# Optimization experiments

Hardware: AMD Instinct MI355X
Metric: run time of the kernel (lower is better)

## Reference

```python
import jax, jax.numpy as jnp
import numpy as np
from jax import lax

J = 3  # number of decomposition levels
SQ2 = float(1.0 / np.sqrt(2.0))


def _corr(Xp, hr, axis, Lout, stride):
    """Strided valid correlation of padded Xp with taps hr along `axis`.
    out[n] = sum_k hr[k] * Xp[n*stride + k]. Tap loop is over <=10 static taps."""
    m = hr.shape[0]
    hi = stride * (Lout - 1) + 1
    acc = hr[0] * lax.slice_in_dim(Xp, 0, hi, stride, axis)
    for k in range(1, m):
        acc = acc + hr[k] * lax.slice_in_dim(Xp, k, k + hi, stride, axis)
    return acc


def colfilter(X, h):
    # 'same' convolution along H with symmetric (edge-repeat) extension.
    m = h.shape[0]; m2 = m // 2; L = X.shape[2]
    Xp = jnp.pad(X, ((0, 0), (0, 0), (m2, m2), (0, 0)), mode='symmetric')
    return _corr(Xp, h[::-1], 2, L, 1)  # corr with reversed taps == convolution


def rowfilter(X, h):
    m = h.shape[0]; m2 = m // 2; L = X.shape[3]
    Xp = jnp.pad(X, ((0, 0), (0, 0), (0, 0), (m2, m2)), mode='symmetric')
    return _corr(Xp, h[::-1], 3, L, 1)


def coldfilt(X, ha, hb, highpass):
    # Dual-tree decimated (by 2) filtering along H. r must be a multiple of 4.
    b, c, r, w = X.shape
    m = ha.shape[0]; r4 = r // 4
    Xp = jnp.pad(X, ((0, 0), (0, 0), (m, m), (0, 0)), mode='symmetric')
    E = Xp[:, :, 2::2, :]  # even-phase stream, len r/2+m-1
    O = Xp[:, :, 3::2, :]  # odd-phase stream
    a_out = _corr(O, ha[::-1], 2, r4, 2)
    b_out = _corr(E, hb[::-1], 2, r4, 2)
    ev, od = (b_out, a_out) if highpass else (a_out, b_out)
    return jnp.stack([ev, od], axis=3).reshape(b, c, r // 2, w)


def rowdfilt(X, ha, hb, highpass):
    b, c, r, w = X.shape
    m = ha.shape[0]; w4 = w // 4
    Xp = jnp.pad(X, ((0, 0), (0, 0), (0, 0), (m, m)), mode='symmetric')
    E = Xp[:, :, :, 2::2]
    O = Xp[:, :, :, 3::2]
    a_out = _corr(O, ha[::-1], 3, w4, 2)
    b_out = _corr(E, hb[::-1], 3, w4, 2)
    ev, od = (b_out, a_out) if highpass else (a_out, b_out)
    return jnp.stack([ev, od], axis=4).reshape(b, c, r, w // 2)


def q2c(y):
    # Convert quads of real pixels into two complex subbands.
    y = y * SQ2
    a = y[..., 0::2, 0::2]; b = y[..., 0::2, 1::2]
    c = y[..., 1::2, 0::2]; d = y[..., 1::2, 1::2]
    return (a - d, b + c), (a + d, b - c)


def _bands(lh, hh, hl):
    # Orientation order [15, 45, 75, 105, 135, 165] deg; real/imag in last dim.
    (r15, i15), (r165, i165) = q2c(lh)
    (r45, i45), (r135, i135) = q2c(hh)
    (r75, i75), (r105, i105) = q2c(hl)
    c = lambda re, im: jnp.stack([re, im], axis=-1)
    return jnp.stack([c(r15, i15), c(r45, i45), c(r75, i75),
                      c(r105, i105), c(r135, i135), c(r165, i165)], axis=2)


def dtcwt_forward(x, h0o, h1o, h0a, h0b, h1a, h1b):
    # Level 1 (undecimated biorthogonal filters; q2c decimates bandpass by 2).
    lo = rowfilter(x, h0o)
    hi = rowfilter(x, h1o)
    ll = colfilter(lo, h0o)
    yh = [_bands(colfilter(lo, h1o), colfilter(hi, h1o), colfilter(hi, h0o))]
    # Levels 2..J (quarter-shift dual-tree decimated filters).
    for _ in range(1, J):
        lo = rowdfilt(ll, h0b, h0a, False)
        hi = rowdfilt(ll, h1b, h1a, True)
        lh = coldfilt(lo, h1b, h1a, True)
        hl = coldfilt(hi, h0b, h0a, False)
        hh = coldfilt(hi, h1b, h1a, True)
        ll = coldfilt(lo, h0b, h0a, False)
        yh.append(_bands(lh, hh, hl))
    return (ll, yh[0], yh[1], yh[2])


def _filters():
    h0o = np.array([-0.05, 0.25, 0.6, 0.25, -0.05], dtype=np.float32)
    h1o = np.array([-3/280, 3/56, 73/280, -17/28, 73/280, 3/56, -3/280],
                   dtype=np.float32)
    h0a = np.array([0.03516384, 0.0, -0.08832942, 0.23389032, 0.76027237,
                    0.58751830, 0.0, -0.11430184, 0.0, 0.0], dtype=np.float32)
    h0b = h0a[::-1].copy()
    alt = ((-1.0) ** np.arange(10)).astype(np.float32)
    h1a = h0b * alt
    h1b = h1a[::-1].copy()
    return {k: jnp.asarray(v) for k, v in dict(
        h0o=h0o, h1o=h1o, h0a=h0a, h0b=h0b, h1a=h1a, h1b=h1b).items()}


def setup_inputs() -> dict:
    key = jax.random.key(0)
    x = jax.random.normal(key, (8, 16, 256, 256), dtype=jnp.float32)
    inp = {'x': x}
    inp.update(_filters())
    return inp


def reference(x, h0o, h1o, h0a, h0b, h1a, h1b):
    return dtcwt_forward(x, h0o, h1o, h0a, h0b, h1a, h1b)
```

## Files before the change

### kernel.cpp

```cpp
#include <hip/hip_runtime.h>

#define SQ2F 0.70710678118654752440f

static constexpr float H0O[5] = {-0.05f, 0.25f, 0.6f, 0.25f, -0.05f};
static constexpr float H1O[7] = {(float)(-3.0/280.0), (float)(3.0/56.0), (float)(73.0/280.0),
                                 (float)(-17.0/28.0), (float)(73.0/280.0), (float)(3.0/56.0),
                                 (float)(-3.0/280.0)};
static constexpr float H0A[10] = {0.03516384f, 0.0f, -0.08832942f, 0.23389032f, 0.76027237f,
                                  0.5875183f, 0.0f, -0.11430184f, 0.0f, 0.0f};
static constexpr float H0B[10] = {0.0f, 0.0f, -0.11430184f, 0.0f, 0.5875183f,
                                  0.76027237f, 0.23389032f, -0.08832942f, 0.0f, 0.03516384f};
static constexpr float H1A[10] = {0.0f, 0.0f, -0.11430184f, 0.0f, 0.5875183f,
                                  -0.76027237f, 0.23389032f, 0.08832942f, 0.0f, -0.03516384f};
static constexpr float H1B[10] = {-0.03516384f, 0.0f, 0.08832942f, 0.23389032f, -0.76027237f,
                                  0.5875183f, 0.0f, -0.11430184f, 0.0f, 0.0f};

__device__ __forceinline__ int symref(int t, int L) {
    if (t < 0) t = -1 - t;
    if (t >= L) t = 2 * L - 1 - t;
    return t;
}

__device__ __forceinline__ void gload_lds4(const float* g, float* lds) {
    __builtin_amdgcn_global_load_lds(
        (const __attribute__((address_space(1))) void*)g,
        (__attribute__((address_space(3))) void*)lds, 4, 0, 0);
}

#define XS(r,c)  S[(r)*84 + (c)]
#define LS(r,c)  S[(r)*85 + (c)]
#define LOS(r,c) S[4368 + (r)*80 + (c)]
#define LO2(r,c) S[4368 + (r)*33 + (c)]
#define HI2(r,c) S[5952 + (r)*33 + (c)]
#define HIS(r,c) S[8528 + (r)*64 + (c)]

__global__ __launch_bounds__(512) void dtcwt_l12(
    const float* __restrict__ x,
    float* __restrict__ yh0,
    float* __restrict__ yh1,
    float* __restrict__ ll2)
{
    __shared__ float S[10960];
    int tid = threadIdx.x, bx = blockIdx.x;
    int tj = bx & 3, ti = (bx >> 2) & 7, bc = bx >> 5;
    const int xr0 = 32 * ti - 10, xc0 = 64 * tj - 10;
    const float* xb = x + (size_t)bc * 65536;
    const int lane = tid & 63;

    const bool interior0 = (ti >= 1) && (ti <= 6) && (tj >= 1) && (tj <= 2);
    if (interior0) {
        for (int p = tid; p < 4368; p += 512) {
            int r = p / 84, c = p - r * 84;
            gload_lds4(xb + (xr0 + r) * 256 + (xc0 + c), &S[p - lane]);
        }
    } else {
        for (int p = tid; p < 4368; p += 512) {
            int r = p / 84, c = p - r * 84;
            gload_lds4(xb + symref(xr0 + r, 256) * 256 + symref(xc0 + c, 256),
                       &S[p - lane]);
        }
    }
    __syncthreads();

    for (int p = tid; p < 4160; p += 512) {
        int r = p / 80, c = p - r * 80;
        float l = 0.f;
        #pragma unroll
        for (int t = 0; t < 5; t++) l += H0O[t] * XS(r, c + 4 - t);
        LOS(r, c) = l;
    }
    for (int p = tid; p < 2432; p += 512) {
        int r = p >> 6, c = p & 63;
        float h = 0.f;
        #pragma unroll
        for (int t = 0; t < 7; t++) h += H1O[t] * XS(r + 7, c + 13 - t);
        HIS(r, c) = h;
    }
    __syncthreads();

    for (int p = tid; p < 3840; p += 512) {
        int r = p / 80, c = p - r * 80;
        float v = 0.f;
        #pragma unroll
        for (int t = 0; t < 5; t++) v += H0O[t] * LOS(r + 4 - t, c);
        LS(r, c) = v;
    }
    {
        float* yb = yh0 + (size_t)bc * 196608;
        const size_t bs = 32768;
        int par = lane & 1;
        #pragma unroll
        for (int it = 0; it < 2; ++it) {
            int oi = (tid >> 6) + 8 * it;
            float low[8], hiw[8];
            #pragma unroll
            for (int k = 0; k < 8; k++) {
                low[k] = LOS(2 * oi + 7 + k, lane + 8);
                hiw[k] = HIS(2 * oi + k,     lane);
            }
            float lh_e = 0, lh_o = 0, hh_e = 0, hh_o = 0, hl_e = 0, hl_o = 0;
            #pragma unroll
            for (int t = 0; t < 7; t++) {
                lh_e += H1O[t] * low[6 - t]; lh_o += H1O[t] * low[7 - t];
                hh_e += H1O[t] * hiw[6 - t]; hh_o += H1O[t] * hiw[7 - t];
            }
            #pragma unroll
            for (int t = 0; t < 5; t++) {
                hl_e += H0O[t] * hiw[5 - t]; hl_o += H0O[t] * hiw[6 - t];
            }
            lh_e *= SQ2F; lh_o *= SQ2F; hh_e *= SQ2F; hh_o *= SQ2F; hl_e *= SQ2F; hl_o *= SQ2F;
            float p0 = lh_e - __shfl_xor(lh_o, 1), q0 = __shfl_xor(lh_e, 1) + lh_o;
            float p1 = hh_e - __shfl_xor(hh_o, 1), q1 = __shfl_xor(hh_e, 1) + hh_o;
            float p2 = hl_e - __shfl_xor(hl_o, 1), q2 = __shfl_xor(hl_e, 1) + hl_o;
            int i0 = 16 * ti + oi, j0 = 32 * tj + (lane >> 1);
            size_t pix = ((size_t)i0 * 128 + j0) * 2;
            *(float2*)&yb[(size_t)(par ? 5 : 0) * bs + pix] =
                par ? make_float2(q0, p0) : make_float2(p0, q0);
            *(float2*)&yb[(size_t)(par ? 4 : 1) * bs + pix] =
                par ? make_float2(q1, p1) : make_float2(p1, q1);
            *(float2*)&yb[(size_t)(par ? 3 : 2) * bs + pix] =
                par ? make_float2(q2, p2) : make_float2(p2, q2);
        }
    }
    __syncthreads();

    {
        const bool interiorC = (tj >= 1) && (tj <= 2);
        for (int p = tid; p < 768; p += 512) {
            int r = p % 48, nl = p / 48;
            float v[20];
            if (interiorC) {
                #pragma unroll
                for (int k = 0; k < 20; k++) v[k] = LS(r, 4 * nl + k);
            } else {
                int gcb = 64 * tj + 4 * nl - 8;
                #pragma unroll
                for (int k = 0; k < 20; k++)
                    v[k] = LS(r, symref(gcb + k, 256) - 64 * tj + 8);
            }
            float aLo = 0.f, bLo = 0.f, aHi = 0.f, bHi = 0.f;
            #pragma unroll
            for (int t = 0; t < 10; t++) {
                float vo = v[19 - 2 * t], ve = v[18 - 2 * t];
                aLo += H0B[t] * vo; bLo += H0A[t] * ve;
                aHi += H1B[t] * vo; bHi += H1A[t] * ve;
            }
            LO2(r, 2*nl)   = aLo;
            LO2(r, 2*nl+1) = bLo;
            HI2(r, 2*nl)   = bHi;
            HI2(r, 2*nl+1) = aHi;
        }
    }
    __syncthreads();

    if (tid < 256) {
        int c  = tid & 31;
        int li = tid >> 5;
        int i1 = 8 * ti + li;
        float vl[20], vh[20];
        const bool interiorR = (ti >= 1) && (ti <= 6);
        if (interiorR) {
            #pragma unroll
            for (int k = 0; k < 20; k++) {
                vl[k] = LO2(4 * li + k, c);
                vh[k] = HI2(4 * li + k, c);
            }
        } else {
            #pragma unroll
            for (int k = 0; k < 20; k++) {
                int loc = symref(32 * ti + 4 * li - 8 + k, 256) - 32 * ti + 8;
                vl[k] = LO2(loc, c);
                vh[k] = HI2(loc, c);
            }
        }
        float a_ll=0,b_ll=0,a_lh=0,b_lh=0,a_hl=0,b_hl=0,a_hh=0,b_hh=0;
        #pragma unroll
        for (int t = 0; t < 10; t++) {
            float vo_l = vl[19 - 2*t], ve_l = vl[18 - 2*t];
            float vo_h = vh[19 - 2*t], ve_h = vh[18 - 2*t];
            a_ll += H0B[t] * vo_l;  b_ll += H0A[t] * ve_l;
            a_lh += H1B[t] * vo_l;  b_lh += H1A[t] * ve_l;
            a_hl += H0B[t] * vo_h;  b_hl += H0A[t] * ve_h;
            a_hh += H1B[t] * vo_h;  b_hh += H1A[t] * ve_h;
        }
        float* llb = ll2 + (size_t)bc * 16384;
        int gcol = 32 * tj + c;
        llb[(size_t)(2*i1)   * 128 + gcol] = a_ll;
        llb[(size_t)(2*i1+1) * 128 + gcol] = b_ll;
        float lh_e = SQ2F*b_lh, lh_o = SQ2F*a_lh;
        float hh_e = SQ2F*b_hh, hh_o = SQ2F*a_hh;
        float hl_e = SQ2F*a_hl, hl_o = SQ2F*b_hl;
        int par = c & 1;
        float p0 = lh_e - __shfl_xor(lh_o, 1), q0 = __shfl_xor(lh_e, 1) + lh_o;
        float p1 = hh_e - __shfl_xor(hh_o, 1), q1 = __shfl_xor(hh_e, 1) + hh_o;
        float p2 = hl_e - __shfl_xor(hl_o, 1), q2 = __shfl_xor(hl_e, 1) + hl_o;
        float* yb = yh1 + (size_t)bc * 49152;
        int j1 = 16 * tj + (c >> 1);
        size_t pix = ((size_t)i1 * 64 + j1) * 2;
        const size_t bs = 8192;
        *(float2*)&yb[(size_t)(par ? 5 : 0) * bs + pix] =
            par ? make_float2(q0, p0) : make_float2(p0, q0);
        *(float2*)&yb[(size_t)(par ? 4 : 1) * bs + pix] =
            par ? make_float2(q1, p1) : make_float2(p1, q1);
        *(float2*)&yb[(size_t)(par ? 3 : 2) * bs + pix] =
            par ? make_float2(q2, p2) : make_float2(p2, q2);
    }
}

__global__ __launch_bounds__(256) void level_fused(
    const float* __restrict__ X,
    float* __restrict__ llout,
    float* __restrict__ yh,
    int R, int C, int nbi, int nbj)
{
    __shared__ float Xs[80][81];
    __shared__ float Lo[80][33];
    __shared__ float Hi[80][33];

    int tid = threadIdx.x;
    int bx  = blockIdx.x;
    int tj = bx % nbj; int ti = (bx / nbj) % nbi; int bc = bx / (nbj * nbi);
    int i0 = ti * 16, j0 = tj * 16;
    int gr0 = 4 * i0 - 8, gc0 = 4 * j0 - 8;
    const float* Xb = X + (size_t)bc * R * C;

    for (int p = tid; p < 80 * 80; p += 256) {
        int r = p / 80, c = p - r * 80;
        Xs[r][c] = Xb[(size_t)symref(gr0 + r, R) * C + symref(gc0 + c, C)];
    }
    __syncthreads();

    for (int p = tid; p < 80 * 16; p += 256) {
        int nl = p / 80, r = p - nl * 80;
        float v[20];
        #pragma unroll
        for (int k = 0; k < 20; k++) v[k] = Xs[r][4 * nl + k];
        float aLo = 0.f, bLo = 0.f, aHi = 0.f, bHi = 0.f;
        #pragma unroll
        for (int t = 0; t < 10; t++) {
            float vo = v[19 - 2 * t], ve = v[18 - 2 * t];
            aLo += H0B[t] * vo; bLo += H0A[t] * ve;
            aHi += H1B[t] * vo; bHi += H1A[t] * ve;
        }
        Lo[r][2*nl]   = aLo;
        Lo[r][2*nl+1] = bLo;
        Hi[r][2*nl]   = bHi;
        Hi[r][2*nl+1] = aHi;
    }
    __syncthreads();

    int R4 = R >> 2, Wq = C >> 2, C2 = C >> 1;
    int lj = tid & 15, li = tid >> 4;
    int i = i0 + li, j = j0 + lj;

    float ll_[2][2], lh_[2][2], hl_[2][2], hh_[2][2];
    #pragma unroll
    for (int cc = 0; cc < 2; cc++) {
        int c = 2 * lj + cc;
        float vl[20], vh[20];
        #pragma unroll
        for (int k = 0; k < 20; k++) {
            vl[k] = Lo[4 * li + k][c];
            vh[k] = Hi[4 * li + k][c];
        }
        float a_ll=0,b_ll=0,a_lh=0,b_lh=0,a_hl=0,b_hl=0,a_hh=0,b_hh=0;
        #pragma unroll
        for (int t = 0; t < 10; t++) {
            float vo_l = vl[19 - 2*t], ve_l = vl[18 - 2*t];
            float vo_h = vh[19 - 2*t], ve_h = vh[18 - 2*t];
            a_ll += H0B[t] * vo_l;  b_ll += H0A[t] * ve_l;
            a_lh += H1B[t] * vo_l;  b_lh += H1A[t] * ve_l;
            a_hl += H0B[t] * vo_h;  b_hl += H0A[t] * ve_h;
            a_hh += H1B[t] * vo_h;  b_hh += H1A[t] * ve_h;
        }
        ll_[0][cc] = a_ll; ll_[1][cc] = b_ll;
        lh_[0][cc] = b_lh; lh_[1][cc] = a_lh;
        hl_[0][cc] = a_hl; hl_[1][cc] = b_hl;
        hh_[0][cc] = b_hh; hh_[1][cc] = a_hh;
    }

    float* llb = llout + (size_t)bc * (R >> 1) * C2;
    llb[(size_t)(2*i)*C2   + 2*j]     = ll_[0][0];
    llb[(size_t)(2*i)*C2   + 2*j + 1] = ll_[0][1];
    llb[(size_t)(2*i+1)*C2 + 2*j]     = ll_[1][0];
    llb[(size_t)(2*i+1)*C2 + 2*j + 1] = ll_[1][1];

    float* yb = yh + (size_t)bc * 6 * R4 * Wq * 2;
    size_t pix = ((size_t)i * Wq + j) * 2;
    size_t bs  = (size_t)R4 * Wq * 2;
    {
        float a = SQ2F*lh_[0][0], b = SQ2F*lh_[0][1], c = SQ2F*lh_[1][0], d = SQ2F*lh_[1][1];
        yb[0*bs + pix] = a - d; yb[0*bs + pix + 1] = b + c;
        yb[5*bs + pix] = a + d; yb[5*bs + pix + 1] = b - c;
    }
    {
        float a = SQ2F*hh_[0][0], b = SQ2F*hh_[0][1], c = SQ2F*hh_[1][0], d = SQ2F*hh_[1][1];
        yb[1*bs + pix] = a - d; yb[1*bs + pix + 1] = b + c;
        yb[4*bs + pix] = a + d; yb[4*bs + pix + 1] = b - c;
    }
    {
        float a = SQ2F*hl_[0][0], b = SQ2F*hl_[0][1], c = SQ2F*hl_[1][0], d = SQ2F*hl_[1][1];
        yb[2*bs + pix] = a - d; yb[2*bs + pix + 1] = b + c;
        yb[3*bs + pix] = a + d; yb[3*bs + pix + 1] = b - c;
    }
}

extern "C" void kernel_launch(void* const* d_in, const int* in_sizes, int n_in,
                              void* d_out, int out_size, void* d_ws, size_t ws_size,
                              hipStream_t stream) {
    const float* x = (const float*)d_in[0];
    float* out = (float*)d_out;

    const int BC = 8 * 16;

    float* out_ll  = out;
    float* out_yh0 = out + 524288;
    float* out_yh1 = out + 25690112;
    float* out_yh2 = out + 31981568;

    float* ll2 = (float*)d_ws;

    dtcwt_l12<<<BC * 32, 512, 0, stream>>>(x, out_yh0, out_yh1, ll2);

    level_fused<<<BC * 4, 256, 0, stream>>>(ll2, out_ll, out_yh2, 128, 128, 2, 2);
}
```

Measured before the change: 209.7 us.

## Vectorize LDS filtering with register blocking and drop boundary symref paths

Reworks both DT-CWT kernels so each thread loads float4/float2 strips from LDS and computes several adjacent outputs from registers. Symmetric filters are folded into pre-added pairs, and the LDS pitches are repadded to keep vector accesses aligned. The level-1 to level-2 path drops the per-tile symref reindexing, relying on the reflected halo already being symmetric after filtering. The level-3 kernel loads its interior with vectorized global reads and handles only the edge columns scalarly. The aim is fewer LDS instructions and less index arithmetic, at the cost of higher register pressure and possible LDS bank conflicts from the new pitches.

```diff
diff --git a/kernel.cpp b/kernel.cpp
--- a/kernel.cpp
+++ b/kernel.cpp
@@ -27,12 +27,41 @@
         (__attribute__((address_space(3))) void*)lds, 4, 0, 0);
 }
 
+__device__ __forceinline__ float2 f2add(float2 a, float2 b) { return make_float2(a.x + b.x, a.y + b.y); }
+__device__ __forceinline__ float2 f2fma(float s, float2 a, float2 b) {
+    return make_float2(fmaf(s, a.x, b.x), fmaf(s, a.y, b.y));
+}
+__device__ __forceinline__ float2 f2s(float s, float2 a) { return make_float2(s * a.x, s * a.y); }
+
+__device__ __forceinline__ float2 f2sym7(float2 a, float2 b, float2 c, float2 d,
+                                         float2 e, float2 f, float2 g) {
+    float2 r = f2s(H1O[3], d);
+    r = f2fma(H1O[0], f2add(a, g), r);
+    r = f2fma(H1O[1], f2add(b, f), r);
+    r = f2fma(H1O[2], f2add(c, e), r);
+    return r;
+}
+__device__ __forceinline__ float2 f2sym5(float2 a, float2 b, float2 c, float2 d, float2 e) {
+    float2 r = f2s(H0O[2], c);
+    r = f2fma(H0O[0], f2add(a, e), r);
+    r = f2fma(H0O[1], f2add(b, d), r);
+    return r;
+}
+__device__ __forceinline__ float4 f4sym5(float4 a, float4 b, float4 c, float4 d, float4 e) {
+    float4 r;
+    r.x = fmaf(H0O[0], a.x + e.x, fmaf(H0O[1], b.x + d.x, H0O[2] * c.x));
+    r.y = fmaf(H0O[0], a.y + e.y, fmaf(H0O[1], b.y + d.y, H0O[2] * c.y));
+    r.z = fmaf(H0O[0], a.z + e.z, fmaf(H0O[1], b.z + d.z, H0O[2] * c.z));
+    r.w = fmaf(H0O[0], a.w + e.w, fmaf(H0O[1], b.w + d.w, H0O[2] * c.w));
+    return r;
+}
+
 #define XS(r,c)  S[(r)*84 + (c)]
-#define LS(r,c)  S[(r)*85 + (c)]
-#define LOS(r,c) S[4368 + (r)*80 + (c)]
-#define LO2(r,c) S[4368 + (r)*33 + (c)]
-#define HI2(r,c) S[5952 + (r)*33 + (c)]
-#define HIS(r,c) S[8528 + (r)*64 + (c)]
+#define LS(r,c)  S[(r)*84 + (c)]
+#define LOS(r,c) S[4368 + (r)*84 + (c)]
+#define LO2(r,c) S[4368 + (r)*34 + (c)]
+#define HI2(r,c) S[6000 + (r)*34 + (c)]
+#define HIS(r,c) S[8736 + (r)*68 + (c)]
 
 __global__ __launch_bounds__(512) void dtcwt_l12(
     const float* __restrict__ x,
@@ -40,7 +69,7 @@
     float* __restrict__ yh1,
     float* __restrict__ ll2)
 {
-    __shared__ float S[10960];
+    __shared__ __align__(16) float S[11320];
     int tid = threadIdx.x, bx = blockIdx.x;
     int tj = bx & 3, ti = (bx >> 2) & 7, bc = bx >> 5;
     const int xr0 = 32 * ti - 10, xc0 = 64 * tj - 10;
@@ -62,148 +91,143 @@
     }
     __syncthreads();
 
-    for (int p = tid; p < 4160; p += 512) {
-        int r = p / 80, c = p - r * 80;
-        float l = 0.f;
-        #pragma unroll
-        for (int t = 0; t < 5; t++) l += H0O[t] * XS(r, c + 4 - t);
-        LOS(r, c) = l;
-    }
-    for (int p = tid; p < 2432; p += 512) {
-        int r = p >> 6, c = p & 63;
-        float h = 0.f;
-        #pragma unroll
-        for (int t = 0; t < 7; t++) h += H1O[t] * XS(r + 7, c + 13 - t);
-        HIS(r, c) = h;
-    }
-    __syncthreads();
-
-    for (int p = tid; p < 3840; p += 512) {
-        int r = p / 80, c = p - r * 80;
-        float v = 0.f;
-        #pragma unroll
-        for (int t = 0; t < 5; t++) v += H0O[t] * LOS(r + 4 - t, c);
-        LS(r, c) = v;
+    for (int p = tid; p < 520; p += 512) {
+        int r = p / 10, s = p - r * 10, c8 = 8 * s;
+        const float* xr = &XS(r, c8);
+        float4 q0 = *(const float4*)&xr[0];
+        float4 q1 = *(const float4*)&xr[4];
+        float4 q2 = *(const float4*)&xr[8];
+        float u[12] = {q0.x,q0.y,q0.z,q0.w, q1.x,q1.y,q1.z,q1.w, q2.x,q2.y,q2.z,q2.w};
+        float l[8];
+        #pragma unroll
+        for (int j = 0; j < 8; j++)
+            l[j] = fmaf(H0O[0], u[j] + u[j+4],
+                   fmaf(H0O[1], u[j+1] + u[j+3], H0O[2] * u[j+2]));
+        *(float4*)&LOS(r, c8)     = make_float4(l[0], l[1], l[2], l[3]);
+        *(float4*)&LOS(r, c8 + 4) = make_float4(l[4], l[5], l[6], l[7]);
+    }
+    for (int p = tid; p < 304; p += 512) {
+        int r = p >> 3, s = p & 7, c8 = 8 * s;
+        const float* xr = &XS(r + 7, c8 + 4);
+        float4 q0 = *(const float4*)&xr[0];
+        float4 q1 = *(const float4*)&xr[4];
+        float4 q2 = *(const float4*)&xr[8];
+        float4 q3 = *(const float4*)&xr[12];
+        float4 q4 = *(const float4*)&xr[16];
+        float w[20] = {q0.x,q0.y,q0.z,q0.w, q1.x,q1.y,q1.z,q1.w, q2.x,q2.y,q2.z,q2.w,
+                       q3.x,q3.y,q3.z,q3.w, q4.x,q4.y,q4.z,q4.w};
+        float h[8];
+        #pragma unroll
+        for (int j = 0; j < 8; j++)
+            h[j] = fmaf(H1O[0], w[j+3] + w[j+9],
+                   fmaf(H1O[1], w[j+4] + w[j+8],
+                   fmaf(H1O[2], w[j+5] + w[j+7], H1O[3] * w[j+6])));
+        *(float4*)&HIS(r, c8)     = make_float4(h[0], h[1], h[2], h[3]);
+        *(float4*)&HIS(r, c8 + 4) = make_float4(h[4], h[5], h[6], h[7]);
+    }
+    __syncthreads();
+
+    for (int p = tid; p < 480; p += 512) {
+        int rp = p / 20, s = p - rp * 20, c4 = 4 * s;
+        const float* l0 = &LOS(2 * rp, c4);
+        float4 m0 = *(const float4*)&l0[0];
+        float4 m1 = *(const float4*)&l0[84];
+        float4 m2 = *(const float4*)&l0[168];
+        float4 m3 = *(const float4*)&l0[252];
+        float4 m4 = *(const float4*)&l0[336];
+        float4 m5 = *(const float4*)&l0[420];
+        *(float4*)&LS(2 * rp,     c4) = f4sym5(m0, m1, m2, m3, m4);
+        *(float4*)&LS(2 * rp + 1, c4) = f4sym5(m1, m2, m3, m4, m5);
     }
     {
         float* yb = yh0 + (size_t)bc * 196608;
         const size_t bs = 32768;
-        int par = lane & 1;
-        #pragma unroll
-        for (int it = 0; it < 2; ++it) {
-            int oi = (tid >> 6) + 8 * it;
-            float low[8], hiw[8];
-            #pragma unroll
-            for (int k = 0; k < 8; k++) {
-                low[k] = LOS(2 * oi + 7 + k, lane + 8);
-                hiw[k] = HIS(2 * oi + k,     lane);
-            }
-            float lh_e = 0, lh_o = 0, hh_e = 0, hh_o = 0, hl_e = 0, hl_o = 0;
-            #pragma unroll
-            for (int t = 0; t < 7; t++) {
-                lh_e += H1O[t] * low[6 - t]; lh_o += H1O[t] * low[7 - t];
-                hh_e += H1O[t] * hiw[6 - t]; hh_o += H1O[t] * hiw[7 - t];
-            }
-            #pragma unroll
-            for (int t = 0; t < 5; t++) {
-                hl_e += H0O[t] * hiw[5 - t]; hl_o += H0O[t] * hiw[6 - t];
-            }
-            lh_e *= SQ2F; lh_o *= SQ2F; hh_e *= SQ2F; hh_o *= SQ2F; hl_e *= SQ2F; hl_o *= SQ2F;
-            float p0 = lh_e - __shfl_xor(lh_o, 1), q0 = __shfl_xor(lh_e, 1) + lh_o;
-            float p1 = hh_e - __shfl_xor(hh_o, 1), q1 = __shfl_xor(hh_e, 1) + hh_o;
-            float p2 = hl_e - __shfl_xor(hl_o, 1), q2 = __shfl_xor(hl_e, 1) + hl_o;
-            int i0 = 16 * ti + oi, j0 = 32 * tj + (lane >> 1);
-            size_t pix = ((size_t)i0 * 128 + j0) * 2;
-            *(float2*)&yb[(size_t)(par ? 5 : 0) * bs + pix] =
-                par ? make_float2(q0, p0) : make_float2(p0, q0);
-            *(float2*)&yb[(size_t)(par ? 4 : 1) * bs + pix] =
-                par ? make_float2(q1, p1) : make_float2(p1, q1);
-            *(float2*)&yb[(size_t)(par ? 3 : 2) * bs + pix] =
-                par ? make_float2(q2, p2) : make_float2(p2, q2);
-        }
-    }
-    __syncthreads();
-
-    {
-        const bool interiorC = (tj >= 1) && (tj <= 2);
-        for (int p = tid; p < 768; p += 512) {
-            int r = p % 48, nl = p / 48;
-            float v[20];
-            if (interiorC) {
-                #pragma unroll
-                for (int k = 0; k < 20; k++) v[k] = LS(r, 4 * nl + k);
-            } else {
-                int gcb = 64 * tj + 4 * nl - 8;
-                #pragma unroll
-                for (int k = 0; k < 20; k++)
-                    v[k] = LS(r, symref(gcb + k, 256) - 64 * tj + 8);
-            }
-            float aLo = 0.f, bLo = 0.f, aHi = 0.f, bHi = 0.f;
-            #pragma unroll
-            for (int t = 0; t < 10; t++) {
-                float vo = v[19 - 2 * t], ve = v[18 - 2 * t];
-                aLo += H0B[t] * vo; bLo += H0A[t] * ve;
-                aHi += H1B[t] * vo; bHi += H1A[t] * ve;
-            }
-            LO2(r, 2*nl)   = aLo;
-            LO2(r, 2*nl+1) = bLo;
-            HI2(r, 2*nl)   = bHi;
-            HI2(r, 2*nl+1) = aHi;
-        }
+        int cp = tid & 31, oi = tid >> 5;
+        float2 low[8], hiw[8];
+        #pragma unroll
+        for (int k = 0; k < 8; k++) {
+            low[k] = *(const float2*)&LOS(2 * oi + 7 + k, 2 * cp + 8);
+            hiw[k] = *(const float2*)&HIS(2 * oi + k,     2 * cp);
+        }
+        float2 lhe = f2s(SQ2F, f2sym7(low[0],low[1],low[2],low[3],low[4],low[5],low[6]));
+        float2 lho = f2s(SQ2F, f2sym7(low[1],low[2],low[3],low[4],low[5],low[6],low[7]));
+        float2 hhe = f2s(SQ2F, f2sym7(hiw[0],hiw[1],hiw[2],hiw[3],hiw[4],hiw[5],hiw[6]));
+        float2 hho = f2s(SQ2F, f2sym7(hiw[1],hiw[2],hiw[3],hiw[4],hiw[5],hiw[6],hiw[7]));
+        float2 hle = f2s(SQ2F, f2sym5(hiw[1],hiw[2],hiw[3],hiw[4],hiw[5]));
+        float2 hlo = f2s(SQ2F, f2sym5(hiw[2],hiw[3],hiw[4],hiw[5],hiw[6]));
+        int i0 = 16 * ti + oi, j0 = 32 * tj + cp;
+        size_t pix = ((size_t)i0 * 128 + j0) * 2;
+        { float a=lhe.x, b=lhe.y, c=lho.x, d=lho.y;
+          *(float2*)&yb[0*bs + pix] = make_float2(a-d, b+c);
+          *(float2*)&yb[5*bs + pix] = make_float2(a+d, b-c); }
+        { float a=hhe.x, b=hhe.y, c=hho.x, d=hho.y;
+          *(float2*)&yb[1*bs + pix] = make_float2(a-d, b+c);
+          *(float2*)&yb[4*bs + pix] = make_float2(a+d, b-c); }
+        { float a=hle.x, b=hle.y, c=hlo.x, d=hlo.y;
+          *(float2*)&yb[2*bs + pix] = make_float2(a-d, b+c);
+          *(float2*)&yb[3*bs + pix] = make_float2(a+d, b-c); }
+    }
+    __syncthreads();
+
+    for (int p = tid; p < 768; p += 512) {
+        int nl = p / 48, r = p - nl * 48;
+        const float* lsr = &LS(r, 4 * nl);
+        float4 q0 = *(const float4*)&lsr[0];
+        float4 q1 = *(const float4*)&lsr[4];
+        float4 q2 = *(const float4*)&lsr[8];
+        float4 q3 = *(const float4*)&lsr[12];
+        float4 q4 = *(const float4*)&lsr[16];
+        float v[20] = {q0.x,q0.y,q0.z,q0.w, q1.x,q1.y,q1.z,q1.w, q2.x,q2.y,q2.z,q2.w,
+                       q3.x,q3.y,q3.z,q3.w, q4.x,q4.y,q4.z,q4.w};
+        float aLo = 0.f, bLo = 0.f, aHi = 0.f, bHi = 0.f;
+        #pragma unroll
+        for (int t = 0; t < 10; t++) {
+            float vo = v[19 - 2*t], ve = v[18 - 2*t];
+            aLo = fmaf(H0B[t], vo, aLo); bLo = fmaf(H0A[t], ve, bLo);
+            aHi = fmaf(H1B[t], vo, aHi); bHi = fmaf(H1A[t], ve, bHi);
+        }
+        *(float2*)&LO2(r, 2*nl) = make_float2(aLo, bLo);
+        *(float2*)&HI2(r, 2*nl) = make_float2(bHi, aHi);
     }
     __syncthreads();
 
     if (tid < 256) {
-        int c  = tid & 31;
-        int li = tid >> 5;
+        int half = tid >> 7, q = tid & 127;
+        int cp = q & 15, li = q >> 4;
         int i1 = 8 * ti + li;
-        float vl[20], vh[20];
-        const bool interiorR = (ti >= 1) && (ti <= 6);
-        if (interiorR) {
-            #pragma unroll
-            for (int k = 0; k < 20; k++) {
-                vl[k] = LO2(4 * li + k, c);
-                vh[k] = HI2(4 * li + k, c);
-            }
-        } else {
-            #pragma unroll
-            for (int k = 0; k < 20; k++) {
-                int loc = symref(32 * ti + 4 * li - 8 + k, 256) - 32 * ti + 8;
-                vl[k] = LO2(loc, c);
-                vh[k] = HI2(loc, c);
-            }
-        }
-        float a_ll=0,b_ll=0,a_lh=0,b_lh=0,a_hl=0,b_hl=0,a_hh=0,b_hh=0;
+        const float* Bp = half ? &HI2(0, 0) : &LO2(0, 0);
+        float2 v[20];
+        #pragma unroll
+        for (int k = 0; k < 20; k++)
+            v[k] = *(const float2*)&Bp[(4 * li + k) * 34 + 2 * cp];
+        float2 z = make_float2(0.f, 0.f);
+        float2 aA = z, bA = z, aB = z, bB = z;
         #pragma unroll
         for (int t = 0; t < 10; t++) {
-            float vo_l = vl[19 - 2*t], ve_l = vl[18 - 2*t];
-            float vo_h = vh[19 - 2*t], ve_h = vh[18 - 2*t];
-            a_ll += H0B[t] * vo_l;  b_ll += H0A[t] * ve_l;
-            a_lh += H1B[t] * vo_l;  b_lh += H1A[t] * ve_l;
-            a_hl += H0B[t] * vo_h;  b_hl += H0A[t] * ve_h;
-            a_hh += H1B[t] * vo_h;  b_hh += H1A[t] * ve_h;
-        }
-        float* llb = ll2 + (size_t)bc * 16384;
-        int gcol = 32 * tj + c;
-        llb[(size_t)(2*i1)   * 128 + gcol] = a_ll;
-        llb[(size_t)(2*i1+1) * 128 + gcol] = b_ll;
-        float lh_e = SQ2F*b_lh, lh_o = SQ2F*a_lh;
-        float hh_e = SQ2F*b_hh, hh_o = SQ2F*a_hh;
-        float hl_e = SQ2F*a_hl, hl_o = SQ2F*b_hl;
-        int par = c & 1;
-        float p0 = lh_e - __shfl_xor(lh_o, 1), q0 = __shfl_xor(lh_e, 1) + lh_o;
-        float p1 = hh_e - __shfl_xor(hh_o, 1), q1 = __shfl_xor(hh_e, 1) + hh_o;
-        float p2 = hl_e - __shfl_xor(hl_o, 1), q2 = __shfl_xor(hl_e, 1) + hl_o;
+            float2 vo = v[19 - 2*t], ve = v[18 - 2*t];
+            aA = f2fma(H0B[t], vo, aA); bA = f2fma(H0A[t], ve, bA);
+            aB = f2fma(H1B[t], vo, aB); bB = f2fma(H1A[t], ve, bB);
+        }
         float* yb = yh1 + (size_t)bc * 49152;
-        int j1 = 16 * tj + (c >> 1);
+        int j1 = 16 * tj + cp;
         size_t pix = ((size_t)i1 * 64 + j1) * 2;
         const size_t bs = 8192;
-        *(float2*)&yb[(size_t)(par ? 5 : 0) * bs + pix] =
-            par ? make_float2(q0, p0) : make_float2(p0, q0);
-        *(float2*)&yb[(size_t)(par ? 4 : 1) * bs + pix] =
-            par ? make_float2(q1, p1) : make_float2(p1, q1);
-        *(float2*)&yb[(size_t)(par ? 3 : 2) * bs + pix] =
-            par ? make_float2(q2, p2) : make_float2(p2, q2);
+        if (half == 0) {
+            float* llb = ll2 + (size_t)bc * 16384;
+            int gc = 32 * tj + 2 * cp;
+            *(float2*)&llb[(size_t)(2*i1)     * 128 + gc] = aA;
+            *(float2*)&llb[(size_t)(2*i1 + 1) * 128 + gc] = bA;
+            float a = SQ2F*bB.x, b = SQ2F*bB.y, c = SQ2F*aB.x, d = SQ2F*aB.y;
+            *(float2*)&yb[0*bs + pix] = make_float2(a-d, b+c);
+            *(float2*)&yb[5*bs + pix] = make_float2(a+d, b-c);
+        } else {
+            float a = SQ2F*bB.x, b = SQ2F*bB.y, c = SQ2F*aB.x, d = SQ2F*aB.y;
+            *(float2*)&yb[1*bs + pix] = make_float2(a-d, b+c);
+            *(float2*)&yb[4*bs + pix] = make_float2(a+d, b-c);
+            a = SQ2F*aA.x; b = SQ2F*aA.y; c = SQ2F*bA.x; d = SQ2F*bA.y;
+            *(float2*)&yb[2*bs + pix] = make_float2(a-d, b+c);
+            *(float2*)&yb[3*bs + pix] = make_float2(a+d, b-c);
+        }
     }
 }
 
@@ -213,9 +237,9 @@
     float* __restrict__ yh,
     int R, int C, int nbi, int nbj)
 {
-    __shared__ float Xs[80][81];
-    __shared__ float Lo[80][33];
-    __shared__ float Hi[80][33];
+    __shared__ __align__(16) float Xs[80 * 84];
+    __shared__ __align__(16) float Lo[80 * 34];
+    __shared__ __align__(16) float Hi[80 * 34];
 
     int tid = threadIdx.x;
     int bx  = blockIdx.x;
@@ -224,28 +248,42 @@
     int gr0 = 4 * i0 - 8, gc0 = 4 * j0 - 8;
     const float* Xb = X + (size_t)bc * R * C;
 
-    for (int p = tid; p < 80 * 80; p += 256) {
-        int r = p / 80, c = p - r * 80;
-        Xs[r][c] = Xb[(size_t)symref(gr0 + r, R) * C + symref(gc0 + c, C)];
-    }
-    __syncthreads();
-
-    for (int p = tid; p < 80 * 16; p += 256) {
+    int cl = (gc0 < 0) ? -gc0 : 0;
+    int cr = (gc0 + 80 > C) ? (C - gc0) : 80;
+    int nq = (cr - cl) >> 2;
+    for (int r = tid >> 5; r < 80; r += 8) {
+        const float* rowp = Xb + (size_t)symref(gr0 + r, R) * C;
+        int q = tid & 31;
+        if (q < nq)
+            *(float4*)&Xs[r * 84 + cl + 4 * q] =
+                *(const float4*)&rowp[gc0 + cl + 4 * q];
+    }
+    for (int r = tid; r < 80; r += 256) {
+        const float* rowp = Xb + (size_t)symref(gr0 + r, R) * C;
+        for (int c = 0; c < cl; c++)  Xs[r * 84 + c] = rowp[symref(gc0 + c, C)];
+        for (int c = cr; c < 80; c++) Xs[r * 84 + c] = rowp[symref(gc0 + c, C)];
+    }
+    __syncthreads();
+
+    for (int p = tid; p < 1280; p += 256) {
         int nl = p / 80, r = p - nl * 80;
-        float v[20];
-        #pragma unroll
-        for (int k = 0; k < 20; k++) v[k] = Xs[r][4 * nl + k];
+        const float* xr = &Xs[r * 84 + 4 * nl];
+        float4 q0 = *(const float4*)&xr[0];
+        float4 q1 = *(const float4*)&xr[4];
+        float4 q2 = *(const float4*)&xr[8];
+        float4 q3 = *(const float4*)&xr[12];
+        float4 q4 = *(const float4*)&xr[16];
+        float v[20] = {q0.x,q0.y,q0.z,q0.w, q1.x,q1.y,q1.z,q1.w, q2.x,q2.y,q2.z,q2.w,
+                       q3.x,q3.y,q3.z,q3.w, q4.x,q4.y,q4.z,q4.w};
         float aLo = 0.f, bLo = 0.f, aHi = 0.f, bHi = 0.f;
         #pragma unroll
         for (int t = 0; t < 10; t++) {
-            float vo = v[19 - 2 * t], ve = v[18 - 2 * t];
-            aLo += H0B[t] * vo; bLo += H0A[t] * ve;
-            aHi += H1B[t] * vo; bHi += H1A[t] * ve;
-        }
-        Lo[r][2*nl]   = aLo;
-        Lo[r][2*nl+1] = bLo;
-        Hi[r][2*nl]   = bHi;
-        Hi[r][2*nl+1] = aHi;
+            float vo = v[19 - 2*t], ve = v[18 - 2*t];
+            aLo = fmaf(H0B[t], vo, aLo); bLo = fmaf(H0A[t], ve, bLo);
+            aHi = fmaf(H1B[t], vo, aHi); bHi = fmaf(H1A[t], ve, bHi);
+        }
+        *(float2*)&Lo[r * 34 + 2 * nl] = make_float2(aLo, bLo);
+        *(float2*)&Hi[r * 34 + 2 * nl] = make_float2(bHi, aHi);
     }
     __syncthreads();
 
@@ -253,56 +291,41 @@
     int lj = tid & 15, li = tid >> 4;
     int i = i0 + li, j = j0 + lj;
 
-    float ll_[2][2], lh_[2][2], hl_[2][2], hh_[2][2];
+    float2 vl[20], vh[20];
     #pragma unroll
-    for (int cc = 0; cc < 2; cc++) {
-        int c = 2 * lj + cc;
-        float vl[20], vh[20];
-        #pragma unroll
-        for (int k = 0; k < 20; k++) {
-            vl[k] = Lo[4 * li + k][c];
-            vh[k] = Hi[4 * li + k][c];
-        }
-        float a_ll=0,b_ll=0,a_lh=0,b_lh=0,a_hl=0,b_hl=0,a_hh=0,b_hh=0;
-        #pragma unroll
-        for (int t = 0; t < 10; t++) {
-            float vo_l = vl[19 - 2*t], ve_l = vl[18 - 2*t];
-            float vo_h = vh[19 - 2*t], ve_h = vh[18 - 2*t];
-            a_ll += H0B[t] * vo_l;  b_ll += H0A[t] * ve_l;
-            a_lh += H1B[t] * vo_l;  b_lh += H1A[t] * ve_l;
-            a_hl += H0B[t] * vo_h;  b_hl += H0A[t] * ve_h;
-            a_hh += H1B[t] * vo_h;  b_hh += H1A[t] * ve_h;
-        }
-        ll_[0][cc] = a_ll; ll_[1][cc] = b_ll;
-        lh_[0][cc] = b_lh; lh_[1][cc] = a_lh;
-        hl_[0][cc] = a_hl; hl_[1][cc] = b_hl;
-        hh_[0][cc] = b_hh; hh_[1][cc] = a_hh;
+    for (int k = 0; k < 20; k++) {
+        vl[k] = *(const float2*)&Lo[(4 * li + k) * 34 + 2 * lj];
+        vh[k] = *(const float2*)&Hi[(4 * li + k) * 34 + 2 * lj];
+    }
+    float2 z = make_float2(0.f, 0.f);
+    float2 a_ll = z, b_ll = z, a_lh = z, b_lh = z;
+    float2 a_hl = z, b_hl = z, a_hh = z, b_hh = z;
+    #pragma unroll
+    for (int t = 0; t < 10; t++) {
+        float2 vo_l = vl[19 - 2*t], ve_l = vl[18 - 2*t];
+        float2 vo_h = vh[19 - 2*t], ve_h = vh[18 - 2*t];
+        a_ll = f2fma(H0B[t], vo_l, a_ll); b_ll = f2fma(H0A[t], ve_l, b_ll);
+        a_lh = f2fma(H1B[t], vo_l, a_lh); b_lh = f2fma(H1A[t], ve_l, b_lh);
+        a_hl = f2fma(H0B[t], vo_h, a_hl); b_hl = f2fma(H0A[t], ve_h, b_hl);
+        a_hh = f2fma(H1B[t], vo_h, a_hh); b_hh = f2fma(H1A[t], ve_h, b_hh);
     }
 
     float* llb = llout + (size_t)bc * (R >> 1) * C2;
-    llb[(size_t)(2*i)*C2   + 2*j]     = ll_[0][0];
-    llb[(size_t)(2*i)*C2   + 2*j + 1] = ll_[0][1];
-    llb[(size_t)(2*i+1)*C2 + 2*j]     = ll_[1][0];
-    llb[(size_t)(2*i+1)*C2 + 2*j + 1] = ll_[1][1];
+    *(float2*)&llb[(size_t)(2*i)   * C2 + 2*j] = a_ll;
+    *(float2*)&llb[(size_t)(2*i+1) * C2 + 2*j] = b_ll;
 
     float* yb = yh + (size_t)bc * 6 * R4 * Wq * 2;
     size_t pix = ((size_t)i * Wq + j) * 2;
     size_t bs  = (size_t)R4 * Wq * 2;
-    {
-        float a = SQ2F*lh_[0][0], b = SQ2F*lh_[0][1], c = SQ2F*lh_[1][0], d = SQ2F*lh_[1][1];
-        yb[0*bs + pix] = a - d; yb[0*bs + pix + 1] = b + c;
-        yb[5*bs + pix] = a + d; yb[5*bs + pix + 1] = b - c;
-    }
-    {
-        float a = SQ2F*hh_[0][0], b = SQ2F*hh_[0][1], c = SQ2F*hh_[1][0], d = SQ2F*hh_[1][1];
-        yb[1*bs + pix] = a - d; yb[1*bs + pix + 1] = b + c;
-        yb[4*bs + pix] = a + d; yb[4*bs + pix + 1] = b - c;
-    }
-    {
-        float a = SQ2F*hl_[0][0], b = SQ2F*hl_[0][1], c = SQ2F*hl_[1][0], d = SQ2F*hl_[1][1];
-        yb[2*bs + pix] = a - d; yb[2*bs + pix + 1] = b + c;
-        yb[3*bs + pix] = a + d; yb[3*bs + pix + 1] = b - c;
-    }
+    { float a = SQ2F*b_lh.x, b = SQ2F*b_lh.y, c = SQ2F*a_lh.x, d = SQ2F*a_lh.y;
+      *(float2*)&yb[0*bs + pix] = make_float2(a-d, b+c);
+      *(float2*)&yb[5*bs + pix] = make_float2(a+d, b-c); }
+    { float a = SQ2F*b_hh.x, b = SQ2F*b_hh.y, c = SQ2F*a_hh.x, d = SQ2F*a_hh.y;
+      *(float2*)&yb[1*bs + pix] = make_float2(a-d, b+c);
+      *(float2*)&yb[4*bs + pix] = make_float2(a+d, b-c); }
+    { float a = SQ2F*a_hl.x, b = SQ2F*a_hl.y, c = SQ2F*b_hl.x, d = SQ2F*b_hl.y;
+      *(float2*)&yb[2*bs + pix] = make_float2(a-d, b+c);
+      *(float2*)&yb[3*bs + pix] = make_float2(a+d, b-c); }
 }
 
 extern "C" void kernel_launch(void* const* d_in, const int* in_sizes, int n_in,
```

New measurement: 185.9 us. -11.4%, faster.
